# Performance work log

Hardware: AMD Instinct MI355X
Metric: run time of the kernel (lower is better)

## Reference

```python
import jax, jax.numpy as jnp
import numpy as np

COMMITMENT_COST = 0.1


def setup_inputs() -> dict:
    key = jax.random.key(0)
    k1, k2 = jax.random.split(key)
    B, D, T, K = 8, 256, 2048, 8192
    z = jax.random.normal(k1, (B, D, T), dtype=jnp.float32)
    # nn.init.uniform_(weight, -1/dim, 1/dim)
    codebook = jax.random.uniform(k2, (K, D), dtype=jnp.float32,
                                  minval=-1.0 / D, maxval=1.0 / D)
    return {"z": z, "codebook": codebook}


def reference(z, codebook):
    B, D, T = z.shape
    # (B*T, D)
    z_flat = jnp.transpose(z, (0, 2, 1)).reshape(B * T, D)
    # squared euclidean distances to each codebook entry: (B*T, K)
    d = (jnp.sum(z_flat * z_flat, axis=1, keepdims=True)
         - 2.0 * (z_flat @ codebook.T)
         + jnp.sum(codebook * codebook, axis=1)[None, :])
    indices = jnp.argmin(d, axis=1)                      # (B*T,)
    z_q = codebook[indices].reshape(B, T, D)             # gather
    z_q = jnp.transpose(z_q, (0, 2, 1))                  # (B, D, T)

    codebook_loss = jnp.mean((z_q - jax.lax.stop_gradient(z)) ** 2)
    commitment_loss = COMMITMENT_COST * jnp.mean(
        (jax.lax.stop_gradient(z_q) - z) ** 2)
    loss = codebook_loss + commitment_loss

    # straight-through estimator
    z_q_st = z + jax.lax.stop_gradient(z_q - z)
    return z_q_st, indices.reshape(B, T), loss
```

## Files before the change

kernel.cpp:

```cpp
#include <hip/hip_runtime.h>
#include <hip/hip_bf16.h>
#include <float.h>
#include <math.h>

#define Bz 8
#define Dd 256
#define Tt 2048
#define Kk 8192
#define Mm (Bz*Tt)

#define NSPL 32

#define ZG_CAP 4096
#define DUMP_CAP (ZG_CAP * NSPL)

#define RESCAN_MARGIN 6e-4f

typedef __attribute__((ext_vector_type(8))) _Float16 f16x8;
typedef __attribute__((ext_vector_type(4))) float    f32x4;

__device__ __forceinline__ void gld16(const void* g, void* l) {
  __builtin_amdgcn_global_load_lds(
      (const __attribute__((address_space(1))) void*)g,
      (__attribute__((address_space(3))) void*)l, 16, 0, 0);
}

__device__ __forceinline__ float np_sumsq128(const float* __restrict__ x) {
  float r0 = __fmul_rn(x[0], x[0]);
  float r1 = __fmul_rn(x[1], x[1]);
  float r2 = __fmul_rn(x[2], x[2]);
  float r3 = __fmul_rn(x[3], x[3]);
  float r4 = __fmul_rn(x[4], x[4]);
  float r5 = __fmul_rn(x[5], x[5]);
  float r6 = __fmul_rn(x[6], x[6]);
  float r7 = __fmul_rn(x[7], x[7]);
  for (int i = 8; i < 128; i += 8) {
    r0 = __fadd_rn(r0, __fmul_rn(x[i+0], x[i+0]));
    r1 = __fadd_rn(r1, __fmul_rn(x[i+1], x[i+1]));
    r2 = __fadd_rn(r2, __fmul_rn(x[i+2], x[i+2]));
    r3 = __fadd_rn(r3, __fmul_rn(x[i+3], x[i+3]));
    r4 = __fadd_rn(r4, __fmul_rn(x[i+4], x[i+4]));
    r5 = __fadd_rn(r5, __fmul_rn(x[i+5], x[i+5]));
    r6 = __fadd_rn(r6, __fmul_rn(x[i+6], x[i+6]));
    r7 = __fadd_rn(r7, __fmul_rn(x[i+7], x[i+7]));
  }
  return __fadd_rn(__fadd_rn(__fadd_rn(r0, r1), __fadd_rn(r2, r3)),
                   __fadd_rn(__fadd_rn(r4, r5), __fadd_rn(r6, r7)));
}
__device__ __forceinline__ float np_sumsq256(const float* __restrict__ x) {
  return __fadd_rn(np_sumsq128(x), np_sumsq128(x + 128));
}

__global__ void k_pre(const float* __restrict__ z, const float* __restrict__ cb,
                      _Float16* __restrict__ Ah, _Float16* __restrict__ Bh,
                      float* __restrict__ sc,
                      double* __restrict__ loss_accum, int* __restrict__ rc) {
  const int bid = blockIdx.x;
  const int tid = threadIdx.x;
  if (bid < 1024) {
    __shared__ _Float16 tile[64][64 + 8];
    const int b  = bid >> 7;
    const int dt = (bid >> 5) & 3;
    const int tt = bid & 31;
    const int d0 = dt * 64, t0 = tt * 64;
    const float* zb = z + ((size_t)b * Dd + d0) * Tt + t0;
    #pragma unroll
    for (int p = 0; p < 4; ++p) {
      const int d  = p * 16 + (tid >> 4);
      const int tl = (tid & 15) * 4;
      const float4 v = *(const float4*)(zb + (size_t)d * Tt + tl);
      tile[tl+0][d] = (_Float16)v.x;
      tile[tl+1][d] = (_Float16)v.y;
      tile[tl+2][d] = (_Float16)v.z;
      tile[tl+3][d] = (_Float16)v.w;
    }
    __syncthreads();
    const int r = tid >> 2, seg = tid & 3;
    const int m = b * Tt + t0 + r;
    int4* dst = (int4*)(Ah + (size_t)m * Dd + d0 + seg * 16);
    const int4* srcv = (const int4*)(&tile[r][seg * 16]);
    dst[0] = srcv[0];
    dst[1] = srcv[1];
  } else if (bid < 2048) {
    const size_t g = (size_t)(bid - 1024) * 256 + tid;
    const float4 v0 = *(const float4*)(cb + g * 8);
    const float4 v1 = *(const float4*)(cb + g * 8 + 4);
    f16x8 o;
    o[0] = (_Float16)(v0.x * 256.f); o[1] = (_Float16)(v0.y * 256.f);
    o[2] = (_Float16)(v0.z * 256.f); o[3] = (_Float16)(v0.w * 256.f);
    o[4] = (_Float16)(v1.x * 256.f); o[5] = (_Float16)(v1.y * 256.f);
    o[6] = (_Float16)(v1.z * 256.f); o[7] = (_Float16)(v1.w * 256.f);
    *(f16x8*)(Bh + g * 8) = o;
  } else {
    if (bid == 2048 && tid == 0) {
      *loss_accum = 0.0; rc[0] = 0; rc[1] = 0; rc[2] = 0;
    }
    const int gid = (bid - 2048) * 256 + tid;
    const int lane = gid & 63;
    const int j = lane & 7, sub = lane >> 3;
    const int row = (gid >> 6) * 8 + sub;
    if (row >= Kk) return;
    const float* x = cb + (size_t)row * Dd;
    float c0 = __fmul_rn(x[j], x[j]);
    float c1 = __fmul_rn(x[128 + j], x[128 + j]);
    #pragma unroll
    for (int i = 8; i < 128; i += 8) {
      c0 = __fadd_rn(c0, __fmul_rn(x[j + i], x[j + i]));
      c1 = __fadd_rn(c1, __fmul_rn(x[128 + j + i], x[128 + j + i]));
    }
    #pragma unroll
    for (int off = 1; off <= 4; off <<= 1) {
      c0 = __fadd_rn(c0, __shfl_xor(c0, off));
      c1 = __fadd_rn(c1, __shfl_xor(c1, off));
    }
    if (j == 0) sc[row] = __fadd_rn(c0, c1);
  }
}

__global__ __launch_bounds__(512, 4)
void k_mfma(const _Float16* __restrict__ Ah, const _Float16* __restrict__ Bh,
            const float* __restrict__ sc,
            float* __restrict__ pd1, float* __restrict__ pd2, int* __restrict__ pi1) {
  __shared__ __align__(16) _Float16 As[128 * 64];
  __shared__ __align__(16) _Float16 Bs[256 * 64];
  __shared__ float mr1[512];
  __shared__ float mr2[512];
  __shared__ int   mri[512];

  const int tid  = threadIdx.x;
  const int bx   = blockIdx.x & 31;
  const int by   = blockIdx.x >> 5;
  const int m0   = by * 128, n0 = bx * 256;
  const int w    = tid >> 6, lane = tid & 63;
  const int wy   = w >> 2, wx = w & 3;
  const int l15  = lane & 15, quad = lane >> 4;
  const int lhi  = lane >> 3, llo = lane & 7;
  const int p    = llo ^ lhi;
  const int sw   = l15 & 7;

  f32x4 acc[4][4];
  #pragma unroll
  for (int mi = 0; mi < 4; ++mi)
    #pragma unroll
    for (int ni = 0; ni < 4; ++ni)
      acc[mi][ni] = (f32x4){0.f, 0.f, 0.f, 0.f};

  for (int kc = 0; kc < 4; ++kc) {
    __syncthreads();
    #pragma unroll
    for (int i = 0; i < 2; ++i) {
      const int c  = w * 2 + i;
      const int r8 = c * 8 + lhi;
      gld16(Ah + (size_t)(m0 + r8) * Dd + kc * 64 + p * 8, As + c * 512);
    }
    #pragma unroll
    for (int i = 0; i < 4; ++i) {
      const int c  = w * 4 + i;
      const int r8 = c * 8 + lhi;
      gld16(Bh + (size_t)(n0 + r8) * Dd + kc * 64 + p * 8, Bs + c * 512);
    }
    __syncthreads();
    #pragma unroll
    for (int ks = 0; ks < 2; ++ks) {
      f16x8 af[4], bf[4];
      #pragma unroll
      for (int mi = 0; mi < 4; ++mi)
        af[mi] = *(const f16x8*)(As + (wy*64 + mi*16 + l15) * 64 + (((ks*4 + quad) ^ sw) * 8));
      #pragma unroll
      for (int ni = 0; ni < 4; ++ni)
        bf[ni] = *(const f16x8*)(Bs + (wx*64 + ni*16 + l15) * 64 + (((ks*4 + quad) ^ sw) * 8));
      #pragma unroll
      for (int mi = 0; mi < 4; ++mi)
        #pragma unroll
        for (int ni = 0; ni < 4; ++ni)
          acc[mi][ni] = __builtin_amdgcn_mfma_f32_16x16x32_f16(bf[ni], af[mi], acc[mi][ni], 0, 0, 0);
    }
  }

  float scv[4][4];
  #pragma unroll
  for (int ni = 0; ni < 4; ++ni)
    *(float4*)&scv[ni][0] = *(const float4*)(sc + n0 + wx * 64 + ni * 16 + quad * 4);

  float s1[4], s2[4]; int i1[4];
  #pragma unroll
  for (int mi = 0; mi < 4; ++mi) {
    float a1 = INFINITY, a2 = INFINITY; int ai = 0x7fffffff;
    #pragma unroll
    for (int ni = 0; ni < 4; ++ni)
      #pragma unroll
      for (int r = 0; r < 4; ++r) {
        const float sv = fmaf(-0.0078125f, acc[mi][ni][r], scv[ni][r]);
        const int   k  = n0 + wx * 64 + ni * 16 + quad * 4 + r;
        if (sv < a1) { a2 = a1; a1 = sv; ai = k; }
        else if (sv < a2) a2 = sv;
      }
    s1[mi] = a1; s2[mi] = a2; i1[mi] = ai;
  }

  #pragma unroll
  for (int off = 16; off <= 32; off <<= 1)
    #pragma unroll
    for (int q = 0; q < 4; ++q) {
      const float o1 = __shfl_xor(s1[q], off);
      const float o2 = __shfl_xor(s2[q], off);
      const int   oi = __shfl_xor(i1[q], off);
      const float n2 = fminf(fminf(s2[q], o2), fmaxf(s1[q], o1));
      if (o1 < s1[q] || (o1 == s1[q] && oi < i1[q])) { s1[q] = o1; i1[q] = oi; }
      s2[q] = n2;
    }

  if (quad == 0) {
    #pragma unroll
    for (int mi = 0; mi < 4; ++mi) {
      const int ml = wy * 64 + mi * 16 + l15;
      mr1[ml * 4 + wx] = s1[mi];
      mr2[ml * 4 + wx] = s2[mi];
      mri[ml * 4 + wx] = i1[mi];
    }
  }
  __syncthreads();
  if (tid < 128) {
    float a1 = INFINITY, a2 = INFINITY; int ai = 0x7fffffff;
    #pragma unroll
    for (int x = 0; x < 4; ++x) {
      const float b1 = mr1[tid * 4 + x], b2 = mr2[tid * 4 + x];
      const int   bi = mri[tid * 4 + x];
      if (b1 < a1 || (b1 == a1 && bi < ai)) { a2 = fminf(a1, b2); a1 = b1; ai = bi; }
      else a2 = fminf(a2, b1);
    }
    const size_t o = (size_t)bx * Mm + (size_t)(m0 + tid);
    pd1[o] = a1; pd2[o] = a2; pi1[o] = ai;
  }
}

__global__ void k_combine(const float* __restrict__ pd1, const float* __restrict__ pd2,
                          const int* __restrict__ pi1, int* __restrict__ idxf,
                          int* __restrict__ rc, int* __restrict__ rlist,
                          float* __restrict__ rthr, int* __restrict__ posm,
                          int* __restrict__ slist, float* __restrict__ outIdx) {
  const int m = blockIdx.x * 64 + threadIdx.x;
  if (m >= Mm) return;
  float a1 = INFINITY, a2 = INFINITY; int ai = 0x7fffffff;
  #pragma unroll
  for (int spl = 0; spl < NSPL; ++spl) {
    const size_t o = (size_t)spl * Mm + m;
    const float b1 = pd1[o], b2 = pd2[o]; const int bi = pi1[o];
    if (b1 < a1 || (b1 == a1 && bi < ai)) { a2 = fminf(a1, b2); a1 = b1; ai = bi; }
    else a2 = fminf(a2, b1);
  }
  idxf[m]   = ai;
  outIdx[m] = (float)ai;
  int pos = -1;
  if (a2 - a1 <= RESCAN_MARGIN) {
    const int p = atomicAdd(&rc[0], 1);
    if (p < ZG_CAP) {
      rlist[p] = m;
      rthr[p]  = a1 + RESCAN_MARGIN;
      pos = p;
    } else {
      const int s = atomicAdd(&rc[2], 1); slist[s] = m;
    }
  }
  posm[m] = pos;
}

__global__ void k_gather(const float* __restrict__ z, const int* __restrict__ rc,
                         const int* __restrict__ rlist, float* __restrict__ zg,
                         float* __restrict__ Ag, unsigned long long* __restrict__ pbrow) {
  __shared__ float zr[Dd];
  const int cnt = min(rc[0], ZG_CAP);
  const int tid = threadIdx.x;
  for (int it = blockIdx.x; it < cnt; it += gridDim.x) {
    const int m = rlist[it];
    const int b = m / Tt, t = m & (Tt - 1);
    __syncthreads();
    zr[tid] = z[(size_t)b * Dd * Tt + (size_t)tid * Tt + t];
    __syncthreads();
    zg[(size_t)it * Dd + tid] = zr[tid];
    if (tid < 8) {
      const int j = tid;
      float c0 = __fmul_rn(zr[j], zr[j]);
      float c1 = __fmul_rn(zr[128 + j], zr[128 + j]);
      #pragma unroll
      for (int i = 8; i < 128; i += 8) {
        c0 = __fadd_rn(c0, __fmul_rn(zr[j + i], zr[j + i]));
        c1 = __fadd_rn(c1, __fmul_rn(zr[128 + j + i], zr[128 + j + i]));
      }
      #pragma unroll
      for (int off = 1; off <= 4; off <<= 1) {
        c0 = __fadd_rn(c0, __shfl_xor(c0, off));
        c1 = __fadd_rn(c1, __shfl_xor(c1, off));
      }
      if (j == 0) { Ag[it] = __fadd_rn(c0, c1); pbrow[it] = ~0ull; }
    }
  }
}

__device__ __forceinline__ unsigned long long cand_pack(
    const float* __restrict__ cb, const float* __restrict__ sc,
    const float* __restrict__ zp, const float Az, const int k) {
  const float* __restrict__ cp = cb + (size_t)k * Dd;
  double M8 = 0.0;
  #pragma unroll
  for (int sg = 0; sg < 8; ++sg) {
    double a0 = 0.0, a1 = 0.0, a2 = 0.0, a3 = 0.0;
    #pragma unroll
    for (int j = 0; j < 32; j += 4) {
      const float4 c4 = *(const float4*)(cp + sg * 32 + j);
      const float4 z4 = *(const float4*)(zp + sg * 32 + j);
      a0 = fma((double)c4.x, (double)z4.x, a0);
      a1 = fma((double)c4.y, (double)z4.y, a1);
      a2 = fma((double)c4.z, (double)z4.z, a2);
      a3 = fma((double)c4.w, (double)z4.w, a3);
    }
    M8 += (a0 + a1) + (a2 + a3);
  }
  const float M  = (float)M8;
  const float t1 = __fsub_rn(Az, __fmul_rn(2.0f, M));
  const float dq = __fadd_rn(t1, sc[k]);
  unsigned int fb = __float_as_uint(dq);
  fb = (fb & 0x80000000u) ? ~fb : (fb | 0x80000000u);
  return ((unsigned long long)fb << 32) | (unsigned)k;
}

__global__ __launch_bounds__(256)
void k_rescan_rows(const float* __restrict__ cb, const float* __restrict__ sc,
                   int* __restrict__ rc, const int* __restrict__ rlist,
                   const float* __restrict__ rthr,
                   const float* __restrict__ pd1, const float* __restrict__ pd2,
                   const int* __restrict__ pi1,
                   const float* __restrict__ zg, const float* __restrict__ Ag,
                   int* __restrict__ dlist,
                   unsigned long long* __restrict__ pbrow) {
  const int cnt  = min(rc[0], ZG_CAP);
  const int wv   = threadIdx.x >> 6;
  const int lane = threadIdx.x & 63;
  const int it   = blockIdx.x * 4 + wv;
  if (it >= cnt) return;
  const int   m   = rlist[it];
  const float thr = rthr[it];
  const float Az  = Ag[it];
  const float* __restrict__ zp = zg + (size_t)it * Dd;

  int cand = -1;
  if (lane < NSPL) {
    const size_t o = (size_t)lane * Mm + m;
    const float b1 = pd1[o], b2 = pd2[o];
    if (b2 <= thr) {
      const int dq = atomicAdd(&rc[1], 1);
      if (dq < DUMP_CAP) dlist[dq] = (it << 5) | lane;
    } else if (b1 <= thr) {
      cand = pi1[o];
    }
  }
  if (cand >= 0)
    atomicMin(pbrow + it, cand_pack(cb, sc, zp, Az, cand));
}

__global__ __launch_bounds__(256)
void k_rescan_dumps(const float* __restrict__ cb, const float* __restrict__ sc,
                    const int* __restrict__ rc, const int* __restrict__ dlist,
                    const float* __restrict__ zg, const float* __restrict__ Ag,
                    unsigned long long* __restrict__ pbrow) {
  const int nd = min(rc[1], DUMP_CAP);
  for (int e = blockIdx.x; e < nd; e += gridDim.x) {
    const int ent = dlist[e];
    const int it = ent >> 5, spl = ent & 31;
    const int k  = spl * 256 + threadIdx.x;
    unsigned long long pk =
        cand_pack(cb, sc, zg + (size_t)it * Dd, Ag[it], k);
    #pragma unroll
    for (int off = 16; off; off >>= 1) {
      const unsigned long long o = __shfl_xor(pk, off);
      if (o < pk) pk = o;
    }
    if ((threadIdx.x & 31) == 0) atomicMin(pbrow + it, pk);
  }
}

__global__ void k_rescan_slow(const float* __restrict__ z, const float* __restrict__ cb,
                              const float* __restrict__ sc,
                              const int* __restrict__ rc, const int* __restrict__ slist,
                              int* __restrict__ idxf, float* __restrict__ outIdx) {
  __shared__ float zrow[Dd];
  __shared__ float Ash;
  __shared__ float sval[256];
  __shared__ int   sidx[256];
  const int tid = threadIdx.x;
  const int cnt = rc[2];
  for (int it = blockIdx.x; it < cnt; it += gridDim.x) {
    const int m = slist[it];
    const int b = m / Tt, t = m & (Tt - 1);
    __syncthreads();
    zrow[tid] = z[(size_t)b * Dd * Tt + (size_t)tid * Tt + t];
    __syncthreads();
    if (tid == 0) Ash = np_sumsq256(zrow);
    __syncthreads();
    const float A = Ash;
    float best = INFINITY; int bi = 0x7fffffff;
    for (int k = tid; k < Kk; k += 256) {
      const float* cr = cb + (size_t)k * Dd;
      double a0 = 0.0, a1 = 0.0, a2 = 0.0, a3 = 0.0;
      for (int d = 0; d < Dd; d += 4) {
        const float4 c4 = *(const float4*)(cr + d);
        a0 = fma((double)c4.x, (double)zrow[d+0], a0);
        a1 = fma((double)c4.y, (double)zrow[d+1], a1);
        a2 = fma((double)c4.z, (double)zrow[d+2], a2);
        a3 = fma((double)c4.w, (double)zrow[d+3], a3);
      }
      const float M  = (float)((a0 + a1) + (a2 + a3));
      const float t1 = __fsub_rn(A, __fmul_rn(2.0f, M));
      const float dq = __fadd_rn(t1, sc[k]);
      if (dq < best) { best = dq; bi = k; }
    }
    sval[tid] = best; sidx[tid] = bi;
    __syncthreads();
    for (int off = 128; off; off >>= 1) {
      if (tid < off) {
        if (sval[tid+off] < sval[tid] ||
            (sval[tid+off] == sval[tid] && sidx[tid+off] < sidx[tid])) {
          sval[tid] = sval[tid+off]; sidx[tid] = sidx[tid+off];
        }
      }
      __syncthreads();
    }
    if (tid == 0) { idxf[m] = sidx[0]; outIdx[m] = (float)sidx[0]; }
    __syncthreads();
  }
}

__global__ void k_out(const float* __restrict__ z, const float* __restrict__ cb,
                      const int* __restrict__ idxf, const int* __restrict__ posm,
                      const unsigned long long* __restrict__ pbrow,
                      float* __restrict__ outZ, float* __restrict__ outIdx,
                      double* __restrict__ loss_accum) {
  __shared__ float tile[64][65];
  const int tid = threadIdx.x;
  const int bidx = blockIdx.x;
  const int b  = bidx >> 7;
  const int dt = (bidx >> 5) & 3;
  const int tt = bidx & 31;
  const int d0 = dt * 64, t0 = tt * 64;
  {
    const int r = tid >> 2, seg = tid & 3;
    const int m = b * Tt + t0 + r;
    int idx = idxf[m];
    const int pos = posm[m];
    if (pos >= 0) {
      const unsigned long long pb = pbrow[pos];
      if (pb != ~0ull) {
        idx = (int)(unsigned)(pb & 0xFFFFFFFFull);
        if (seg == 0) outIdx[m] = (float)idx;
      }
    }
    const float* src = cb + (size_t)idx * Dd + d0 + seg * 16;
    #pragma unroll
    for (int q4 = 0; q4 < 4; ++q4) {
      const float4 v = *(const float4*)(src + q4 * 4);
      tile[seg * 16 + q4 * 4 + 0][r] = v.x;
      tile[seg * 16 + q4 * 4 + 1][r] = v.y;
      tile[seg * 16 + q4 * 4 + 2][r] = v.z;
      tile[seg * 16 + q4 * 4 + 3][r] = v.w;
    }
  }
  __syncthreads();
  const float* zbase = z + ((size_t)b * Dd + d0) * Tt + t0;
  float*       obase = outZ + ((size_t)b * Dd + d0) * Tt + t0;
  double ls = 0.0;
  #pragma unroll
  for (int p = 0; p < 4; ++p) {
    const int d  = p * 16 + (tid >> 4);
    const int t4 = (tid & 15) * 4;
    const float4 zv = *(const float4*)(zbase + (size_t)d * Tt + t4);
    const float q0 = tile[d][t4+0], q1 = tile[d][t4+1];
    const float q2 = tile[d][t4+2], q3 = tile[d][t4+3];
    const float r0 = q0 - zv.x, r1 = q1 - zv.y, r2 = q2 - zv.z, r3 = q3 - zv.w;
    float4 o;
    o.x = zv.x + r0; o.y = zv.y + r1; o.z = zv.z + r2; o.w = zv.w + r3;
    *(float4*)(obase + (size_t)d * Tt + t4) = o;
    ls += (double)r0*r0 + (double)r1*r1 + (double)r2*r2 + (double)r3*r3;
  }
  #pragma unroll
  for (int off = 32; off; off >>= 1) ls += __shfl_down(ls, off);
  if ((tid & 63) == 0) atomicAdd(loss_accum, ls);
}

__global__ void k_finalize(const double* __restrict__ loss_accum, float* __restrict__ outLoss) {
  const double mean = *loss_accum / (double)((size_t)Bz * Dd * Tt);
  *outLoss = (float)(mean + 0.1 * mean);
}

extern "C" void kernel_launch(void* const* d_in, const int* in_sizes, int n_in,
                              void* d_out, int out_size, void* d_ws, size_t ws_size,
                              hipStream_t stream) {
  (void)in_sizes; (void)n_in; (void)out_size; (void)ws_size;
  const float* z  = (const float*)d_in[0];
  const float* cb = (const float*)d_in[1];

  float* outZ    = (float*)d_out;
  float* outIdx  = outZ + (size_t)Bz * Dd * Tt;
  float* outLoss = outIdx + Mm;

  char* w = (char*)d_ws;
  double*    loss_accum = (double*)w;    w += 16;
  int*       rc         = (int*)w;       w += 16;
  int*       rlist      = (int*)w;       w += sizeof(int)   * Mm;
  int*       slist      = (int*)w;       w += sizeof(int)   * Mm;
  int*       idxf       = (int*)w;       w += sizeof(int)   * Mm;
  int*       posm       = (int*)w;       w += sizeof(int)   * Mm;
  float*     sc         = (float*)w;     w += sizeof(float) * Kk;
  float*     rthr       = (float*)w;     w += sizeof(float) * ZG_CAP;
  int*       dlist      = (int*)w;       w += sizeof(int)   * DUMP_CAP;
  _Float16*  Ah         = (_Float16*)w;  w += sizeof(_Float16) * (size_t)Mm * Dd;
  _Float16*  Bh         = (_Float16*)w;  w += sizeof(_Float16) * (size_t)Kk * Dd;
  float*     zg         = (float*)w;     w += sizeof(float) * (size_t)ZG_CAP * Dd;
  float*     Ag         = (float*)w;     w += sizeof(float) * ZG_CAP;
  unsigned long long* pbrow = (unsigned long long*)w; w += sizeof(unsigned long long) * ZG_CAP;
  float*     pd1        = (float*)w;     w += sizeof(float) * (size_t)NSPL * Mm;
  float*     pd2        = (float*)w;     w += sizeof(float) * (size_t)NSPL * Mm;
  int*       pi1        = (int*)w;

  k_pre          <<<dim3(2304), 256, 0, stream>>>(z, cb, Ah, Bh, sc, loss_accum, rc);
  k_mfma         <<<dim3((Mm / 128) * (Kk / 256)), 512, 0, stream>>>(Ah, Bh, sc, pd1, pd2, pi1);
  k_combine      <<<dim3(Mm / 64), 64, 0, stream>>>(pd1, pd2, pi1, idxf, rc, rlist, rthr, posm, slist, outIdx);
  k_gather       <<<dim3(256), 256, 0, stream>>>(z, rc, rlist, zg, Ag, pbrow);
  k_rescan_rows  <<<dim3(ZG_CAP / 4), 256, 0, stream>>>(cb, sc, rc, rlist, rthr, pd1, pd2, pi1, zg, Ag, dlist, pbrow);
  k_rescan_dumps <<<dim3(256), 256, 0, stream>>>(cb, sc, rc, dlist, zg, Ag, pbrow);
  k_rescan_slow  <<<dim3(64), 256, 0, stream>>>(z, cb, sc, rc, slist, idxf, outIdx);
  k_out          <<<dim3(1024), 256, 0, stream>>>(z, cb, idxf, posm, pbrow, outZ, outIdx, loss_accum);
  k_finalize     <<<dim3(1), 1, 0, stream>>>(loss_accum, outLoss);
}
```

Baseline: 285.2 us.

## Fuse gather kernel into rescan_rows and alias MFMA reduction scratch onto LDS

Removes the separate k_gather launch. Each wave in k_rescan_rows now loads its own z column into shared memory, writes zg, computes the row norm and uses the shared copy for candidate scoring, and k_combine initialises pbrow. Separately, the MFMA kernel's reduction arrays reuse the A tile's shared memory, with an added barrier, to cut LDS footprint and possibly raise occupancy. The risk is an extra barrier in the MFMA epilogue and strided z loads now running inside the rescan kernel.

```diff
diff --git a/kernel.cpp b/kernel.cpp
--- a/kernel.cpp
+++ b/kernel.cpp
@@ -123,9 +123,9 @@
             float* __restrict__ pd1, float* __restrict__ pd2, int* __restrict__ pi1) {
   __shared__ __align__(16) _Float16 As[128 * 64];
   __shared__ __align__(16) _Float16 Bs[256 * 64];
-  __shared__ float mr1[512];
-  __shared__ float mr2[512];
-  __shared__ int   mri[512];
+  float* mr1 = reinterpret_cast<float*>(As);
+  float* mr2 = mr1 + 512;
+  int*   mri = reinterpret_cast<int*>(mr1 + 1024);
 
   const int tid  = threadIdx.x;
   const int bx   = blockIdx.x & 31;
@@ -210,6 +210,7 @@
       s2[q] = n2;
     }
 
+  __syncthreads();
   if (quad == 0) {
     #pragma unroll
     for (int mi = 0; mi < 4; ++mi) {
@@ -238,7 +239,8 @@
                           const int* __restrict__ pi1, int* __restrict__ idxf,
                           int* __restrict__ rc, int* __restrict__ rlist,
                           float* __restrict__ rthr, int* __restrict__ posm,
-                          int* __restrict__ slist, float* __restrict__ outIdx) {
+                          int* __restrict__ slist, unsigned long long* __restrict__ pbrow,
+                          float* __restrict__ outIdx) {
   const int m = blockIdx.x * 64 + threadIdx.x;
   if (m >= Mm) return;
   float a1 = INFINITY, a2 = INFINITY; int ai = 0x7fffffff;
@@ -257,6 +259,7 @@
     if (p < ZG_CAP) {
       rlist[p] = m;
       rthr[p]  = a1 + RESCAN_MARGIN;
+      pbrow[p] = ~0ull;
       pos = p;
     } else {
       const int s = atomicAdd(&rc[2], 1); slist[s] = m;
@@ -265,41 +268,9 @@
   posm[m] = pos;
 }
 
-__global__ void k_gather(const float* __restrict__ z, const int* __restrict__ rc,
-                         const int* __restrict__ rlist, float* __restrict__ zg,
-                         float* __restrict__ Ag, unsigned long long* __restrict__ pbrow) {
-  __shared__ float zr[Dd];
-  const int cnt = min(rc[0], ZG_CAP);
-  const int tid = threadIdx.x;
-  for (int it = blockIdx.x; it < cnt; it += gridDim.x) {
-    const int m = rlist[it];
-    const int b = m / Tt, t = m & (Tt - 1);
-    __syncthreads();
-    zr[tid] = z[(size_t)b * Dd * Tt + (size_t)tid * Tt + t];
-    __syncthreads();
-    zg[(size_t)it * Dd + tid] = zr[tid];
-    if (tid < 8) {
-      const int j = tid;
-      float c0 = __fmul_rn(zr[j], zr[j]);
-      float c1 = __fmul_rn(zr[128 + j], zr[128 + j]);
-      #pragma unroll
-      for (int i = 8; i < 128; i += 8) {
-        c0 = __fadd_rn(c0, __fmul_rn(zr[j + i], zr[j + i]));
-        c1 = __fadd_rn(c1, __fmul_rn(zr[128 + j + i], zr[128 + j + i]));
-      }
-      #pragma unroll
-      for (int off = 1; off <= 4; off <<= 1) {
-        c0 = __fadd_rn(c0, __shfl_xor(c0, off));
-        c1 = __fadd_rn(c1, __shfl_xor(c1, off));
-      }
-      if (j == 0) { Ag[it] = __fadd_rn(c0, c1); pbrow[it] = ~0ull; }
-    }
-  }
-}
-
 __device__ __forceinline__ unsigned long long cand_pack(
     const float* __restrict__ cb, const float* __restrict__ sc,
-    const float* __restrict__ zp, const float Az, const int k) {
+    const float* zp, const float Az, const int k) {
   const float* __restrict__ cp = cb + (size_t)k * Dd;
   double M8 = 0.0;
   #pragma unroll
@@ -325,24 +296,58 @@
 }
 
 __global__ __launch_bounds__(256)
-void k_rescan_rows(const float* __restrict__ cb, const float* __restrict__ sc,
+void k_rescan_rows(const float* __restrict__ z, const float* __restrict__ cb,
+                   const float* __restrict__ sc,
                    int* __restrict__ rc, const int* __restrict__ rlist,
                    const float* __restrict__ rthr,
                    const float* __restrict__ pd1, const float* __restrict__ pd2,
                    const int* __restrict__ pi1,
-                   const float* __restrict__ zg, const float* __restrict__ Ag,
+                   float* __restrict__ zg, float* __restrict__ Ag,
                    int* __restrict__ dlist,
                    unsigned long long* __restrict__ pbrow) {
+  __shared__ __align__(16) float zrb[4][Dd];
   const int cnt  = min(rc[0], ZG_CAP);
   const int wv   = threadIdx.x >> 6;
   const int lane = threadIdx.x & 63;
   const int it   = blockIdx.x * 4 + wv;
-  if (it >= cnt) return;
-  const int   m   = rlist[it];
+  const bool act = (it < cnt);
+  int m = 0;
+  if (act) {
+    m = rlist[it];
+    const int b = m / Tt, t = m & (Tt - 1);
+    #pragma unroll
+    for (int i = 0; i < 4; ++i) {
+      const int d = i * 64 + lane;
+      const float v = z[(size_t)b * Dd * Tt + (size_t)d * Tt + t];
+      zrb[wv][d] = v;
+      zg[(size_t)it * Dd + d] = v;
+    }
+  }
+  __syncthreads();
+  if (!act) return;
+
+  float c0 = 0.f, c1 = 0.f;
+  if (lane < 8) {
+    const int j = lane;
+    const float* x = zrb[wv];
+    c0 = __fmul_rn(x[j], x[j]);
+    c1 = __fmul_rn(x[128 + j], x[128 + j]);
+    #pragma unroll
+    for (int i = 8; i < 128; i += 8) {
+      c0 = __fadd_rn(c0, __fmul_rn(x[j + i], x[j + i]));
+      c1 = __fadd_rn(c1, __fmul_rn(x[128 + j + i], x[128 + j + i]));
+    }
+  }
+  #pragma unroll
+  for (int off = 1; off <= 4; off <<= 1) {
+    c0 = __fadd_rn(c0, __shfl_xor(c0, off));
+    c1 = __fadd_rn(c1, __shfl_xor(c1, off));
+  }
+  const float AzL = __fadd_rn(c0, c1);
+  const float Az  = __shfl(AzL, 0);
+  if (lane == 0) Ag[it] = Az;
+
   const float thr = rthr[it];
-  const float Az  = Ag[it];
-  const float* __restrict__ zp = zg + (size_t)it * Dd;
-
   int cand = -1;
   if (lane < NSPL) {
     const size_t o = (size_t)lane * Mm + m;
@@ -355,7 +360,7 @@
     }
   }
   if (cand >= 0)
-    atomicMin(pbrow + it, cand_pack(cb, sc, zp, Az, cand));
+    atomicMin(pbrow + it, cand_pack(cb, sc, zrb[wv], Az, cand));
 }
 
 __global__ __launch_bounds__(256)
@@ -523,9 +528,8 @@
 
   k_pre          <<<dim3(2304), 256, 0, stream>>>(z, cb, Ah, Bh, sc, loss_accum, rc);
   k_mfma         <<<dim3((Mm / 128) * (Kk / 256)), 512, 0, stream>>>(Ah, Bh, sc, pd1, pd2, pi1);
-  k_combine      <<<dim3(Mm / 64), 64, 0, stream>>>(pd1, pd2, pi1, idxf, rc, rlist, rthr, posm, slist, outIdx);
-  k_gather       <<<dim3(256), 256, 0, stream>>>(z, rc, rlist, zg, Ag, pbrow);
-  k_rescan_rows  <<<dim3(ZG_CAP / 4), 256, 0, stream>>>(cb, sc, rc, rlist, rthr, pd1, pd2, pi1, zg, Ag, dlist, pbrow);
+  k_combine      <<<dim3(Mm / 64), 64, 0, stream>>>(pd1, pd2, pi1, idxf, rc, rlist, rthr, posm, slist, pbrow, outIdx);
+  k_rescan_rows  <<<dim3(ZG_CAP / 4), 256, 0, stream>>>(z, cb, sc, rc, rlist, rthr, pd1, pd2, pi1, zg, Ag, dlist, pbrow);
   k_rescan_dumps <<<dim3(256), 256, 0, stream>>>(cb, sc, rc, dlist, zg, Ag, pbrow);
   k_rescan_slow  <<<dim3(64), 256, 0, stream>>>(z, cb, sc, rc, slist, idxf, outIdx);
   k_out          <<<dim3(1024), 256, 0, stream>>>(z, cb, idxf, posm, pbrow, outZ, outIdx, loss_accum);
```

After: 278.7 us. -2.3%, faster.
